# Kernel optimization log

Measured on AMD Instinct MI355X. Metric: run time of the kernel, lower is better.

## Reference

```python
import jax, jax.numpy as jnp
import numpy as np

N_NODES = 50000
N_EDGES = 640000
DIMS = [128, 256, 128]


def setup_inputs() -> dict:
    key = jax.random.key(0)
    ks = jax.random.split(key, 8)
    x = jax.random.normal(ks[0], (N_NODES, DIMS[0]), dtype=jnp.float32)
    src = jax.random.randint(ks[1], (N_EDGES,), 0, N_NODES)
    dst = jax.random.randint(ks[2], (N_EDGES,), 0, N_NODES)
    # ensure no pre-existing self loops so add_remaining_self_loops == append all loops
    dst = jnp.where(dst == src, (dst + 1) % N_NODES, dst)
    edge_index = jnp.stack([src, dst]).astype(jnp.int64)
    # SAGEConv lin_l weights (root_weight=False -> only neighbor linear), Kaiming-ish init
    def lin(k, fan_in, fan_out):
        s = 1.0 / np.sqrt(fan_in)
        kw, kb = jax.random.split(k)
        W = jax.random.uniform(kw, (fan_out, fan_in), minval=-s, maxval=s, dtype=jnp.float32)
        b = jax.random.uniform(kb, (fan_out,), minval=-s, maxval=s, dtype=jnp.float32)
        return W, b
    W1, b1 = lin(ks[3], DIMS[0], DIMS[1])
    W2, b2 = lin(ks[4], DIMS[1], DIMS[2])
    logit_scale = jnp.asarray(np.log(1.0 / 0.07), dtype=jnp.float32)
    return {"x": x, "edge_index": edge_index, "W1": W1, "b1": b1,
            "W2": W2, "b2": b2, "logit_scale": logit_scale}


def reference(x, edge_index, W1, b1, W2, b2, logit_scale):
    N = x.shape[0]
    loops = jnp.arange(N, dtype=edge_index.dtype)
    src = jnp.concatenate([edge_index[0], loops])  # add_remaining_self_loops
    dst = jnp.concatenate([edge_index[1], loops])
    deg = jax.ops.segment_sum(jnp.ones_like(dst, dtype=x.dtype), dst, num_segments=N)
    inv_deg = 1.0 / deg  # deg >= 1 thanks to self loops

    def sage_conv(y, W, b):
        # mean aggregation of source features at destination, then linear
        agg = jax.ops.segment_sum(y[src], dst, num_segments=N) * inv_deg[:, None]
        return agg @ W.T + b

    y = jax.nn.relu(sage_conv(x, W1, b1))
    y = sage_conv(y, W2, b2)
    # F.normalize(p=2, dim=-1, eps=1e-12)
    nrm = jnp.maximum(jnp.linalg.norm(y, axis=-1, keepdims=True), 1e-12)
    y = y / nrm
    return y * jnp.exp(logit_scale)
```

## Files before the change

kernel.cpp:

```cpp
#include <hip/hip_runtime.h>
#include <hip/hip_bf16.h>

#define N_NODES 50000
#define NPAD 50048
#define D0 128
#define D1 256
#define D2 128
#define N4 1600000
#define CAP 128

typedef __attribute__((ext_vector_type(8))) short short8;
typedef __attribute__((ext_vector_type(8))) unsigned short ushort8;
typedef __attribute__((ext_vector_type(4))) float f32x4;

static __device__ __forceinline__ unsigned short f2bf(float f) {
    __hip_bfloat16 h = __float2bfloat16(f);
    return *(unsigned short*)&h;
}
static __device__ __forceinline__ float bf2f(unsigned short u) {
    return __uint_as_float(((unsigned int)u) << 16);
}

__global__ __launch_bounds__(256) void k_prep(const float* __restrict__ x,
                                              unsigned short* __restrict__ x_bf,
                                              int* __restrict__ cursor,
                                              const float* __restrict__ W1,
                                              const float* __restrict__ W2,
                                              unsigned short* __restrict__ W1p,
                                              unsigned short* __restrict__ W2p,
                                              const int* __restrict__ ei32,
                                              int* __restrict__ flag) {
    int idx = blockIdx.x * 256 + threadIdx.x;
    if (idx < N4) {
        float4 v = ((const float4*)x)[idx];
        ushort4 u;
        u.x = f2bf(v.x); u.y = f2bf(v.y); u.z = f2bf(v.z); u.w = f2bf(v.w);
        ((ushort4*)x_bf)[idx] = u;
    }
    if (idx < N_NODES) cursor[idx] = 0;
    if (idx < 2 * D0 * D1) {
        if (idx < D0 * D1) {
            int j = idx & 7, lane = (idx >> 3) & 63, tile = idx >> 9;
            int ct = tile & 15, kt = tile >> 4;
            int k = kt * 32 + (lane >> 4) * 8 + j;
            int n = ct * 16 + (lane & 15);
            W1p[idx] = f2bf(W1[n * D0 + k]);
        } else {
            int i2 = idx - D0 * D1;
            int j = i2 & 7, lane = (i2 >> 3) & 63, tile = i2 >> 9;
            int ct = tile & 7, kt = tile >> 3;
            int k = kt * 32 + (lane >> 4) * 8 + j;
            int n = ct * 16 + (lane & 15);
            W2p[i2] = f2bf(W2[n * D1 + k]);
        }
    }
    if (blockIdx.x == gridDim.x - 1 && threadIdx.x < 64) {
        int lane = threadIdx.x;
        int nz = 0;
#pragma unroll
        for (int k = 0; k < 16; k++) nz += (ei32[2 * (lane * 16 + k) + 1] != 0);
#pragma unroll
        for (int off = 32; off > 0; off >>= 1) nz += __shfl_down(nz, off, 64);
        if (lane == 0) *flag = (nz == 0) ? 1 : 0;
    }
}

__global__ __launch_bounds__(256) void k_bucket(const int* __restrict__ ei,
                                                int* __restrict__ cursor,
                                                int* __restrict__ csr, int E,
                                                const int* __restrict__ flag) {
    int i = blockIdx.x * 256 + threadIdx.x;
    if (2 * i >= E) return;
    int is64 = *flag;
    int s0, d0, s1, d1;
    if (is64) {
        int4 sp = ((const int4*)ei)[i];
        int4 dp = ((const int4*)(ei + 2 * (size_t)E))[i];
        s0 = sp.x; s1 = sp.z; d0 = dp.x; d1 = dp.z;
    } else {
        int2 sp = ((const int2*)ei)[i];
        int2 dp = ((const int2*)(ei + (size_t)E))[i];
        s0 = sp.x; s1 = sp.y; d0 = dp.x; d1 = dp.y;
    }
    int p0 = atomicAdd(&cursor[d0], 1);
    if (p0 < CAP) csr[(size_t)d0 * CAP + p0] = s0;
    if (2 * i + 1 < E) {
        int p1 = atomicAdd(&cursor[d1], 1);
        if (p1 < CAP) csr[(size_t)d1 * CAP + p1] = s1;
    }
}

#define A_LD 136
#define H_LD 264
__global__ __launch_bounds__(256) void k_gmlp(const unsigned short* __restrict__ x_bf,
                                              const int* __restrict__ csr,
                                              const int* __restrict__ cursor,
                                              const unsigned short* __restrict__ W1p,
                                              const float* __restrict__ b1,
                                              const unsigned short* __restrict__ W2p,
                                              unsigned short* __restrict__ t_bf) {
    __shared__ unsigned short aL[64 * A_LD];
    __shared__ unsigned short hL[64 * H_LD];
    int tid = threadIdx.x;
    int n0 = blockIdx.x * 64;
    int w = tid >> 6, lane = tid & 63;
    int m = lane & 15, q = lane >> 4;

    {
        int h = lane & 15;
        int sub = lane >> 4;
#pragma unroll
        for (int r = 0; r < 4; r++) {
            int row = w * 16 + r * 4 + sub;
            int node = n0 + row;
            unsigned short* lp = aL + row * A_LD + h * 8;
            if (node < N_NODES) {
                float a0[8], a1[8];
                ushort8 u = *(const ushort8*)(x_bf + (size_t)node * 128 + h * 8);
#pragma unroll
                for (int t = 0; t < 8; t++) { a0[t] = bf2f(u[t]); a1[t] = 0.f; }
                int dg = cursor[node]; if (dg > CAP) dg = CAP;
                const int* cp = csr + (size_t)node * CAP;
                int j = 0;
                for (; j + 4 <= dg; j += 4) {
                    int s0 = cp[j], s1 = cp[j + 1], s2 = cp[j + 2], s3 = cp[j + 3];
                    ushort8 r0 = *(const ushort8*)(x_bf + (size_t)s0 * 128 + h * 8);
                    ushort8 r1 = *(const ushort8*)(x_bf + (size_t)s1 * 128 + h * 8);
                    ushort8 r2 = *(const ushort8*)(x_bf + (size_t)s2 * 128 + h * 8);
                    ushort8 r3 = *(const ushort8*)(x_bf + (size_t)s3 * 128 + h * 8);
#pragma unroll
                    for (int t = 0; t < 8; t++) {
                        a0[t] += bf2f(r0[t]) + bf2f(r1[t]);
                        a1[t] += bf2f(r2[t]) + bf2f(r3[t]);
                    }
                }
                for (; j < dg; j++) {
                    ushort8 rr = *(const ushort8*)(x_bf + (size_t)cp[j] * 128 + h * 8);
#pragma unroll
                    for (int t = 0; t < 8; t++) a0[t] += bf2f(rr[t]);
                }
                float invd = 1.0f / (float)(dg + 1);
                ushort8 o;
#pragma unroll
                for (int t = 0; t < 8; t++) o[t] = f2bf((a0[t] + a1[t]) * invd);
                *(ushort8*)lp = o;
            } else {
                ushort8 z = {0, 0, 0, 0, 0, 0, 0, 0};
                *(ushort8*)lp = z;
            }
        }
    }

    {
        short8 af[4];
        const unsigned short* arow = aL + (w * 16 + m) * A_LD + q * 8;
#pragma unroll
        for (int kt = 0; kt < 4; kt++) af[kt] = *(const short8*)(arow + kt * 32);
#pragma unroll
        for (int ct = 0; ct < 16; ct++) {
            f32x4 acc = {0.f, 0.f, 0.f, 0.f};
#pragma unroll
            for (int kt = 0; kt < 4; kt++) {
                short8 bf = *(const short8*)(W1p + (((kt * 16 + ct) * 64 + lane) << 3));
                acc = __builtin_amdgcn_mfma_f32_16x16x32_bf16(af[kt], bf, acc, 0, 0, 0);
            }
            int c = ct * 16 + m;
            float bias = b1[c];
#pragma unroll
            for (int r = 0; r < 4; r++) {
                float v = fmaxf(acc[r] + bias, 0.0f);
                hL[(w * 16 + q * 4 + r) * H_LD + c] = f2bf(v);
            }
        }
    }

    {
        short8 hf[8];
        const unsigned short* hrow = hL + (w * 16 + m) * H_LD + q * 8;
#pragma unroll
        for (int kt = 0; kt < 8; kt++) hf[kt] = *(const short8*)(hrow + kt * 32);
#pragma unroll
        for (int ct = 0; ct < 8; ct++) {
            f32x4 acc = {0.f, 0.f, 0.f, 0.f};
#pragma unroll
            for (int kt = 0; kt < 8; kt++) {
                short8 bf = *(const short8*)(W2p + (((kt * 8 + ct) * 64 + lane) << 3));
                acc = __builtin_amdgcn_mfma_f32_16x16x32_bf16(hf[kt], bf, acc, 0, 0, 0);
            }
            int c = ct * 16 + m;
#pragma unroll
            for (int r = 0; r < 4; r++) {
                int node = n0 + w * 16 + q * 4 + r;
                if (node < N_NODES) t_bf[(size_t)node * 128 + c] = f2bf(acc[r]);
            }
        }
    }
}

__global__ __launch_bounds__(256) void k_gather_final(const unsigned short* __restrict__ t,
                                                      const int* __restrict__ csr,
                                                      const int* __restrict__ cursor,
                                                      const float* __restrict__ b2,
                                                      const float* __restrict__ ls,
                                                      float* __restrict__ out) {
    int tid = threadIdx.x;
    int h = tid & 15;
    int node = blockIdx.x * 16 + (tid >> 4);

    float a0[8], a1[8];
    ushort8 u = *(const ushort8*)(t + (size_t)node * 128 + h * 8);
#pragma unroll
    for (int k = 0; k < 8; k++) { a0[k] = bf2f(u[k]); a1[k] = 0.f; }
    int dg = cursor[node]; if (dg > CAP) dg = CAP;
    const int* cp = csr + (size_t)node * CAP;
    int j = 0;
    for (; j + 4 <= dg; j += 4) {
        int s0 = cp[j], s1 = cp[j + 1], s2 = cp[j + 2], s3 = cp[j + 3];
        ushort8 r0 = *(const ushort8*)(t + (size_t)s0 * 128 + h * 8);
        ushort8 r1 = *(const ushort8*)(t + (size_t)s1 * 128 + h * 8);
        ushort8 r2 = *(const ushort8*)(t + (size_t)s2 * 128 + h * 8);
        ushort8 r3 = *(const ushort8*)(t + (size_t)s3 * 128 + h * 8);
#pragma unroll
        for (int k = 0; k < 8; k++) {
            a0[k] += bf2f(r0[k]) + bf2f(r1[k]);
            a1[k] += bf2f(r2[k]) + bf2f(r3[k]);
        }
    }
    for (; j < dg; j++) {
        ushort8 rr = *(const ushort8*)(t + (size_t)cp[j] * 128 + h * 8);
#pragma unroll
        for (int k = 0; k < 8; k++) a0[k] += bf2f(rr[k]);
    }
    float invd = 1.0f / (float)(dg + 1);
    float4 bb0 = ((const float4*)b2)[h * 2];
    float4 bb1 = ((const float4*)b2)[h * 2 + 1];
    float v[8];
    v[0] = (a0[0] + a1[0]) * invd + bb0.x;
    v[1] = (a0[1] + a1[1]) * invd + bb0.y;
    v[2] = (a0[2] + a1[2]) * invd + bb0.z;
    v[3] = (a0[3] + a1[3]) * invd + bb0.w;
    v[4] = (a0[4] + a1[4]) * invd + bb1.x;
    v[5] = (a0[5] + a1[5]) * invd + bb1.y;
    v[6] = (a0[6] + a1[6]) * invd + bb1.z;
    v[7] = (a0[7] + a1[7]) * invd + bb1.w;

    float s = 0.f;
#pragma unroll
    for (int k = 0; k < 8; k++) s += v[k] * v[k];
#pragma unroll
    for (int msk = 8; msk > 0; msk >>= 1) s += __shfl_xor(s, msk, 64);
    float nrm = fmaxf(sqrtf(s), 1e-12f);
    float scale = expf(ls[0]) / nrm;
    float4 o0, o1;
    o0.x = v[0] * scale; o0.y = v[1] * scale; o0.z = v[2] * scale; o0.w = v[3] * scale;
    o1.x = v[4] * scale; o1.y = v[5] * scale; o1.z = v[6] * scale; o1.w = v[7] * scale;
    float* op = out + (size_t)node * 128 + h * 8;
    *(float4*)(op + 0) = o0;
    *(float4*)(op + 4) = o1;
}

extern "C" void kernel_launch(void* const* d_in, const int* in_sizes, int n_in,
                              void* d_out, int out_size, void* d_ws, size_t ws_size,
                              hipStream_t stream) {
    const float* x  = (const float*)d_in[0];
    const int*   ei = (const int*)d_in[1];
    const float* W1 = (const float*)d_in[2];
    const float* b1 = (const float*)d_in[3];
    const float* W2 = (const float*)d_in[4];
    const float* b2 = (const float*)d_in[5];
    const float* ls = (const float*)d_in[6];
    float* out = (float*)d_out;

    const int E = in_sizes[1] / 2;

    char* ws = (char*)d_ws;
    size_t off = 0;
    auto alloc = [&](size_t bytes) {
        size_t o = off;
        off = (off + bytes + 255) & ~(size_t)255;
        return o;
    };
    int*            flag   = (int*)(ws + alloc(256));
    int*            cursor = (int*)(ws + alloc((size_t)N_NODES * 4));
    int*            csr    = (int*)(ws + alloc((size_t)N_NODES * CAP * 4));
    unsigned short* W1p    = (unsigned short*)(ws + alloc((size_t)D0 * D1 * 2));
    unsigned short* W2p    = (unsigned short*)(ws + alloc((size_t)D1 * D2 * 2));
    unsigned short* x_bf   = (unsigned short*)(ws + alloc((size_t)N_NODES * D0 * 2));
    unsigned short* t_bf   = (unsigned short*)(ws + alloc((size_t)N_NODES * D2 * 2));

    k_prep<<<N4 / 256, 256, 0, stream>>>(x, x_bf, cursor, W1, W2, W1p, W2p, ei, flag);
    k_bucket<<<(E / 2 + 255) / 256, 256, 0, stream>>>(ei, cursor, csr, E, flag);
    k_gmlp<<<NPAD / 64, 256, 0, stream>>>(x_bf, csr, cursor, W1p, b1, W2p, t_bf);
    k_gather_final<<<N_NODES / 16, 256, 0, stream>>>(t_bf, csr, cursor, b2, ls, out);
}
```

Before: 216.9 us.

## Pad gathers to 8 with zero row and shrink gmlp shared memory

Both gather loops now issue eight independent row loads per iteration, with indices padded to a multiple of eight that point at an all-zero row appended to x_bf and t_bf. This removes the scalar tail loop and raises memory-level parallelism. The k_gmlp kernel reuses a single per-wave LDS buffer for both the aggregated input and the hidden activations, with a smaller stride and a launch-bounds occupancy hint of 4, so more blocks fit per CU. In exchange, low-degree nodes do some wasted loads from the zero row, and register pressure is higher.

```diff
diff --git a/kernel.cpp b/kernel.cpp
--- a/kernel.cpp
+++ b/kernel.cpp
@@ -3,10 +3,12 @@
 
 #define N_NODES 50000
 #define NPAD 50048
+#define ZROW N_NODES
 #define D0 128
 #define D1 256
 #define D2 128
 #define N4 1600000
+#define NB4 1601536
 #define CAP 128
 
 typedef __attribute__((ext_vector_type(8))) short short8;
@@ -36,6 +38,9 @@
         ushort4 u;
         u.x = f2bf(v.x); u.y = f2bf(v.y); u.z = f2bf(v.z); u.w = f2bf(v.w);
         ((ushort4*)x_bf)[idx] = u;
+    } else if (idx < NB4) {
+        ushort4 z = {0, 0, 0, 0};
+        ((ushort4*)x_bf)[idx] = z;
     }
     if (idx < N_NODES) cursor[idx] = 0;
     if (idx < 2 * D0 * D1) {
@@ -90,30 +95,29 @@
     }
 }
 
-#define A_LD 136
-#define H_LD 264
-__global__ __launch_bounds__(256) void k_gmlp(const unsigned short* __restrict__ x_bf,
-                                              const int* __restrict__ csr,
-                                              const int* __restrict__ cursor,
-                                              const unsigned short* __restrict__ W1p,
-                                              const float* __restrict__ b1,
-                                              const unsigned short* __restrict__ W2p,
-                                              unsigned short* __restrict__ t_bf) {
-    __shared__ unsigned short aL[64 * A_LD];
-    __shared__ unsigned short hL[64 * H_LD];
+#define H_LD 260
+__global__ __launch_bounds__(256, 4) void k_gmlp(const unsigned short* __restrict__ x_bf,
+                                                 const int* __restrict__ csr,
+                                                 const int* __restrict__ cursor,
+                                                 const unsigned short* __restrict__ W1p,
+                                                 const float* __restrict__ b1,
+                                                 const unsigned short* __restrict__ W2p,
+                                                 unsigned short* __restrict__ t_bf) {
+    __shared__ unsigned short sbuf[4][16 * H_LD];
     int tid = threadIdx.x;
     int n0 = blockIdx.x * 64;
     int w = tid >> 6, lane = tid & 63;
     int m = lane & 15, q = lane >> 4;
+    unsigned short* wbuf = sbuf[w];
 
     {
         int h = lane & 15;
         int sub = lane >> 4;
 #pragma unroll
         for (int r = 0; r < 4; r++) {
-            int row = w * 16 + r * 4 + sub;
-            int node = n0 + row;
-            unsigned short* lp = aL + row * A_LD + h * 8;
+            int lrow = r * 4 + sub;
+            int node = n0 + w * 16 + lrow;
+            unsigned short* lp = wbuf + lrow * H_LD + h * 8;
             if (node < N_NODES) {
                 float a0[8], a1[8];
                 ushort8 u = *(const ushort8*)(x_bf + (size_t)node * 128 + h * 8);
@@ -121,23 +125,23 @@
                 for (int t = 0; t < 8; t++) { a0[t] = bf2f(u[t]); a1[t] = 0.f; }
                 int dg = cursor[node]; if (dg > CAP) dg = CAP;
                 const int* cp = csr + (size_t)node * CAP;
-                int j = 0;
-                for (; j + 4 <= dg; j += 4) {
-                    int s0 = cp[j], s1 = cp[j + 1], s2 = cp[j + 2], s3 = cp[j + 3];
-                    ushort8 r0 = *(const ushort8*)(x_bf + (size_t)s0 * 128 + h * 8);
-                    ushort8 r1 = *(const ushort8*)(x_bf + (size_t)s1 * 128 + h * 8);
-                    ushort8 r2 = *(const ushort8*)(x_bf + (size_t)s2 * 128 + h * 8);
-                    ushort8 r3 = *(const ushort8*)(x_bf + (size_t)s3 * 128 + h * 8);
+                int jn = (dg + 7) & ~7;
+                for (int j = 0; j < jn; j += 8) {
+                    int idx[8];
+#pragma unroll
+                    for (int u8 = 0; u8 < 8; u8++) {
+                        int jj = j + u8;
+                        idx[u8] = (jj < dg) ? cp[jj] : ZROW;
+                    }
+                    ushort8 rr[8];
+#pragma unroll
+                    for (int u8 = 0; u8 < 8; u8++)
+                        rr[u8] = *(const ushort8*)(x_bf + (size_t)idx[u8] * 128 + h * 8);
 #pragma unroll
                     for (int t = 0; t < 8; t++) {
-                        a0[t] += bf2f(r0[t]) + bf2f(r1[t]);
-                        a1[t] += bf2f(r2[t]) + bf2f(r3[t]);
+                        a0[t] += bf2f(rr[0][t]) + bf2f(rr[2][t]) + bf2f(rr[4][t]) + bf2f(rr[6][t]);
+                        a1[t] += bf2f(rr[1][t]) + bf2f(rr[3][t]) + bf2f(rr[5][t]) + bf2f(rr[7][t]);
                     }
-                }
-                for (; j < dg; j++) {
-                    ushort8 rr = *(const ushort8*)(x_bf + (size_t)cp[j] * 128 + h * 8);
-#pragma unroll
-                    for (int t = 0; t < 8; t++) a0[t] += bf2f(rr[t]);
                 }
                 float invd = 1.0f / (float)(dg + 1);
                 ushort8 o;
@@ -153,7 +157,7 @@
 
     {
         short8 af[4];
-        const unsigned short* arow = aL + (w * 16 + m) * A_LD + q * 8;
+        const unsigned short* arow = wbuf + m * H_LD + q * 8;
 #pragma unroll
         for (int kt = 0; kt < 4; kt++) af[kt] = *(const short8*)(arow + kt * 32);
 #pragma unroll
@@ -169,14 +173,14 @@
 #pragma unroll
             for (int r = 0; r < 4; r++) {
                 float v = fmaxf(acc[r] + bias, 0.0f);
-                hL[(w * 16 + q * 4 + r) * H_LD + c] = f2bf(v);
+                wbuf[(q * 4 + r) * H_LD + c] = f2bf(v);
             }
         }
     }
 
     {
         short8 hf[8];
-        const unsigned short* hrow = hL + (w * 16 + m) * H_LD + q * 8;
+        const unsigned short* hrow = wbuf + m * H_LD + q * 8;
 #pragma unroll
         for (int kt = 0; kt < 8; kt++) hf[kt] = *(const short8*)(hrow + kt * 32);
 #pragma unroll
@@ -191,7 +195,7 @@
 #pragma unroll
             for (int r = 0; r < 4; r++) {
                 int node = n0 + w * 16 + q * 4 + r;
-                if (node < N_NODES) t_bf[(size_t)node * 128 + c] = f2bf(acc[r]);
+                t_bf[(size_t)node * 128 + c] = (node < N_NODES) ? f2bf(acc[r]) : (unsigned short)0;
             }
         }
     }
@@ -213,23 +217,23 @@
     for (int k = 0; k < 8; k++) { a0[k] = bf2f(u[k]); a1[k] = 0.f; }
     int dg = cursor[node]; if (dg > CAP) dg = CAP;
     const int* cp = csr + (size_t)node * CAP;
-    int j = 0;
-    for (; j + 4 <= dg; j += 4) {
-        int s0 = cp[j], s1 = cp[j + 1], s2 = cp[j + 2], s3 = cp[j + 3];
-        ushort8 r0 = *(const ushort8*)(t + (size_t)s0 * 128 + h * 8);
-        ushort8 r1 = *(const ushort8*)(t + (size_t)s1 * 128 + h * 8);
-        ushort8 r2 = *(const ushort8*)(t + (size_t)s2 * 128 + h * 8);
-        ushort8 r3 = *(const ushort8*)(t + (size_t)s3 * 128 + h * 8);
+    int jn = (dg + 7) & ~7;
+    for (int j = 0; j < jn; j += 8) {
+        int idx[8];
+#pragma unroll
+        for (int u8 = 0; u8 < 8; u8++) {
+            int jj = j + u8;
+            idx[u8] = (jj < dg) ? cp[jj] : ZROW;
+        }
+        ushort8 rr[8];
+#pragma unroll
+        for (int u8 = 0; u8 < 8; u8++)
+            rr[u8] = *(const ushort8*)(t + (size_t)idx[u8] * 128 + h * 8);
 #pragma unroll
         for (int k = 0; k < 8; k++) {
-            a0[k] += bf2f(r0[k]) + bf2f(r1[k]);
-            a1[k] += bf2f(r2[k]) + bf2f(r3[k]);
-        }
-    }
-    for (; j < dg; j++) {
-        ushort8 rr = *(const ushort8*)(t + (size_t)cp[j] * 128 + h * 8);
-#pragma unroll
-        for (int k = 0; k < 8; k++) a0[k] += bf2f(rr[k]);
+            a0[k] += bf2f(rr[0][k]) + bf2f(rr[2][k]) + bf2f(rr[4][k]) + bf2f(rr[6][k]);
+            a1[k] += bf2f(rr[1][k]) + bf2f(rr[3][k]) + bf2f(rr[5][k]) + bf2f(rr[7][k]);
+        }
     }
     float invd = 1.0f / (float)(dg + 1);
     float4 bb0 = ((const float4*)b2)[h * 2];
@@ -285,10 +289,10 @@
     int*            csr    = (int*)(ws + alloc((size_t)N_NODES * CAP * 4));
     unsigned short* W1p    = (unsigned short*)(ws + alloc((size_t)D0 * D1 * 2));
     unsigned short* W2p    = (unsigned short*)(ws + alloc((size_t)D1 * D2 * 2));
-    unsigned short* x_bf   = (unsigned short*)(ws + alloc((size_t)N_NODES * D0 * 2));
-    unsigned short* t_bf   = (unsigned short*)(ws + alloc((size_t)N_NODES * D2 * 2));
-
-    k_prep<<<N4 / 256, 256, 0, stream>>>(x, x_bf, cursor, W1, W2, W1p, W2p, ei, flag);
+    unsigned short* x_bf   = (unsigned short*)(ws + alloc((size_t)NPAD * D0 * 2));
+    unsigned short* t_bf   = (unsigned short*)(ws + alloc((size_t)NPAD * D2 * 2));
+
+    k_prep<<<(NB4 + 255) / 256, 256, 0, stream>>>(x, x_bf, cursor, W1, W2, W1p, W2p, ei, flag);
     k_bucket<<<(E / 2 + 255) / 256, 256, 0, stream>>>(ei, cursor, csr, E, flag);
     k_gmlp<<<NPAD / 64, 256, 0, stream>>>(x_bf, csr, cursor, W1p, b1, W2p, t_bf);
     k_gather_final<<<N_NODES / 16, 256, 0, stream>>>(t_bf, csr, cursor, b2, ls, out);
```

After: 210.4 us. -3.0%, faster.
